# Kernel optimization log

Measured on AMD Instinct MI355X. Metric: run time of the kernel, lower is better.

## Reference

```python
import jax, jax.numpy as jnp
import numpy as np

K = 10
ALPHA = 0.1
N_NODES = 100000
N_EDGES = 1600000
D_FEAT = 50


def setup_inputs() -> dict:
    key = jax.random.key(0)
    k1, k2, k3 = jax.random.split(key, 3)
    feat = jax.random.normal(k1, (N_NODES, D_FEAT), dtype=jnp.float32)
    src = jax.random.randint(k2, (N_EDGES,), 0, N_NODES, dtype=jnp.int64)
    dst = jax.random.randint(k3, (N_EDGES,), 0, N_NODES, dtype=jnp.int64)
    return {"feat": feat, "src": src, "dst": dst}


def reference(feat, src, dst):
    # APPNP: H^{t+1} = (1-a) * D^{-1/2} A D^{-1/2} H^t + a * H^0
    n = feat.shape[0]
    # in-degree per node, clipped to >= 1 (as in the original clip_by_value)
    deg = jax.ops.segment_sum(jnp.ones(dst.shape[0], feat.dtype), dst, num_segments=n)
    norm = jnp.clip(deg, 1.0, None) ** -0.5  # [N]
    norm = norm[:, None]                      # broadcast over feature dims
    feat_0 = feat
    for _ in range(K):
        h = feat * norm                       # pre-normalize (D^{-1/2})
        # message = h[src] (edge weight is 1 since edge_drop=0), aggregate by sum at dst
        agg = jax.ops.segment_sum(h[src], dst, num_segments=n)  # [N, D]
        feat = (1.0 - ALPHA) * (agg * norm) + ALPHA * feat_0
    return feat
```

## Files before the change

kernel.cpp:

```cpp
#include <hip/hip_runtime.h>


#define NN 100000
#define EE 1600000
#define DD 50
#define GS 64
#define KK 10
#define NBLK 391
#define PBLK 256
#define PE (EE / PBLK)
#define PR 4
#define NR (NN / PR)
#define CAP 2176
#define SG 32

__device__ __forceinline__ float feat_at(const void* f, long long i, int ft) {
    if (ft) return ((const float*)f)[i];
    unsigned int w = ((unsigned int)((const unsigned short*)f)[i]) << 16;
    return __uint_as_float(w);
}

__device__ __forceinline__ float bf16_ld(const unsigned short* p, int i) {
    unsigned int w = ((unsigned int)p[i]) << 16;
    return __uint_as_float(w);
}

__device__ __forceinline__ unsigned short bf16_st(float x) {
    unsigned int u = __float_as_uint(x);
    unsigned int r = (u + 0x7FFF + ((u >> 16) & 1)) >> 16;
    return (unsigned short)r;
}

__global__ __launch_bounds__(512) void APPNPConv_62199716381208_build(
        const void* srcp, const void* dstp, const void* featp,
        int2* pairs, int* rcnt, unsigned int* counts,
        int* row_ptr, int* col_idx, int* flag, int phase) {
    __shared__ unsigned int hist[NR / 2];
    __shared__ unsigned int cur[PR];
    const int tid = threadIdx.x;

    if (phase == 0) {
        const int sp = blockIdx.x;
        const long long e0 = (long long)sp * PE;
        const int* a = (const int*)dstp;
        const int is64 = ((a[1] | a[3] | a[5] | a[7] | a[9] | a[11] | a[13] | a[15]) == 0);
        if (sp == 0 && tid == 0) {
            flag[0] = is64;
            const unsigned short* w = (const unsigned short*)featp;
            int isf32 = 0;
            for (int k = 0; k < 64; ++k) {
                unsigned int b = ((unsigned int)w[k]) << 16;
                float ax = fabsf(__uint_as_float(b));
                if (!(ax < 100.0f)) isf32 = 1;
            }
            flag[1] = isf32;
        }
        if (tid < PR) cur[tid] = 0u;
        __syncthreads();
        const int lane = tid & 63;
        const unsigned long long lmask = (1ULL << lane) - 1ULL;
        const long long* dst64 = (const long long*)dstp;
        const long long* src64 = (const long long*)srcp;
        const int* dst32 = (const int*)dstp;
        const int* src32 = (const int*)srcp;
        for (int i = tid; i < PE; i += 512) {
            long long e = e0 + i;
            int d, c;
            if (is64) { d = (int)dst64[e]; c = (int)src64[e]; }
            else      { d = dst32[e];      c = src32[e]; }
            int ok = ((unsigned int)d < (unsigned int)NN);
            int cc = ((unsigned int)c < (unsigned int)NN) ? c : 0;
            int r = ok ? (d / NR) : -1;
            #pragma unroll
            for (int rb = 0; rb < PR; ++rb) {
                unsigned long long m = __ballot(r == rb);
                if (m) {
                    int leader = (int)__ffsll((unsigned long long)m) - 1;
                    unsigned int base = 0u;
                    if (lane == leader)
                        base = atomicAdd(&cur[rb], (unsigned int)__popcll(m));
                    base = (unsigned int)__shfl((int)base, leader, 64);
                    if (r == rb) {
                        unsigned int pos = base + (unsigned int)__popcll(m & lmask);
                        if (pos < (unsigned int)CAP)
                            pairs[((sp << 2) + rb) * CAP + pos] = make_int2(d, cc);
                    }
                }
            }
        }
        __syncthreads();
        if (tid < PR) {
            unsigned int v = cur[tid];
            rcnt[(sp << 2) + tid] = (int)(v < (unsigned int)CAP ? v : (unsigned int)CAP);
        }
        return;
    }

    const int r = blockIdx.x & 3;
    const int sg = blockIdx.x >> 2;

    if (phase == 1) {
        for (int i = tid; i < NR / 2; i += 512) hist[i] = 0u;
        __syncthreads();
        #pragma unroll
        for (int k = 0; k < 8; ++k) {
            int sp = (sg << 3) + k;
            int len = rcnt[(sp << 2) + r];
            const int2* pb = pairs + ((sp << 2) + r) * CAP;
            for (int i = tid; i < len; i += 512) {
                int2 pc = pb[i];
                int dloc = pc.x - r * NR;
                atomicAdd(&hist[dloc >> 1], 1u << ((dloc & 1) << 4));
            }
        }
        __syncthreads();
        for (int i = tid; i < NR; i += 512)
            counts[(size_t)sg * NN + r * NR + i] =
                (hist[i >> 1] >> ((i & 1) << 4)) & 0xFFFFu;
        return;
    }

    {
        const unsigned int* cb = counts + (size_t)sg * NN + r * NR;
        for (int i = tid; i < NR / 2; i += 512) {
            unsigned int lo = cb[2 * i];
            unsigned int hi = cb[2 * i + 1];
            hist[i] = (lo & 0xFFFFu) | (hi << 16);
        }
        __syncthreads();
        #pragma unroll
        for (int k = 0; k < 8; ++k) {
            int sp = (sg << 3) + k;
            int len = rcnt[(sp << 2) + r];
            const int2* pb = pairs + ((sp << 2) + r) * CAP;
            for (int i = tid; i < len; i += 512) {
                int2 pc = pb[i];
                int dloc = pc.x - r * NR;
                unsigned int old = atomicAdd(&hist[dloc >> 1], 1u << ((dloc & 1) << 4));
                unsigned int off = (old >> ((dloc & 1) << 4)) & 0xFFFFu;
                unsigned int pos = (unsigned int)row_ptr[pc.x] + off;
                if (pos < (unsigned int)EE) col_idx[pos] = pc.y;
            }
        }
        return;
    }
}

__global__ __launch_bounds__(512) void APPNPConv_62199716381208_kernel(
        const void* featp, const void* srcp, const void* dstp,
        int* deg, float* norm, int* row_ptr, int* col_idx, int* bsum, int* flag,
        unsigned int* counts,
        const unsigned short* gin, unsigned short* gout, float* outp,
        int phase, int last) {
    __shared__ int sh[512];
    const int tid = threadIdx.x;

    if (phase == 2) {
        int n = blockIdx.x * 256 + tid;
        int total = 0;
        if (n < NN) {
            #pragma unroll 4
            for (int s = 0; s < SG; ++s)
                total += (int)counts[(size_t)s * NN + n];
            deg[n] = total;
            norm[n] = rsqrtf((float)(total < 1 ? 1 : total));
        }
        sh[tid] = total;
        __syncthreads();
        for (int off = 128; off > 0; off >>= 1) {
            if (tid < off) sh[tid] += sh[tid + off];
            __syncthreads();
        }
        if (tid == 0) bsum[blockIdx.x] = sh[0];
        return;
    }
    if (phase == 3) {
        int v = (tid < NBLK) ? bsum[tid] : 0;
        sh[tid] = v;
        __syncthreads();
        for (int off = 1; off < 512; off <<= 1) {
            int x = (tid >= off) ? sh[tid - off] : 0;
            __syncthreads();
            sh[tid] += x;
            __syncthreads();
        }
        if (tid < NBLK) bsum[tid] = sh[tid] - v;
        return;
    }
    if (phase == 4) {
        int i = blockIdx.x * 256 + tid;
        int v = (i < NN) ? deg[i] : 0;
        sh[tid] = v;
        __syncthreads();
        for (int off = 1; off < 256; off <<= 1) {
            int x = (tid >= off) ? sh[tid - off] : 0;
            __syncthreads();
            sh[tid] += x;
            __syncthreads();
        }
        int excl = sh[tid] - v + bsum[blockIdx.x];
        if (i < NN) {
            row_ptr[i] = excl;
            unsigned int run = 0u;
            for (int s = 0; s < SG; ++s) {
                size_t o = (size_t)s * NN + i;
                unsigned int c = counts[o];
                counts[o] = run;
                run += c;
            }
        }
        if (i == 0) row_ptr[NN] = EE;
        return;
    }
    if (phase == 6) {
        int gidx = blockIdx.x * 256 + tid;
        int v = gidx >> 6;
        int d = gidx & 63;
        if (v < NN) {
            unsigned short val = 0;
            if (d < DD) {
                float x = feat_at(featp, (long long)v * DD + d, flag[1]);
                val = bf16_st(x * norm[v]);
            }
            gout[(v << 6) + d] = val;
        }
        return;
    }
    {
        const int lane = tid & 63;
        const int nwg = gridDim.x;
        const int xcd = blockIdx.x & 7;
        const int bpos = blockIdx.x >> 3;
        const int q = nwg >> 3, rm = nwg & 7;
        const int sb = (xcd < rm ? xcd * (q + 1) : rm * (q + 1) + (xcd - rm) * q) + bpos;
        const int v = (sb << 2) + (tid >> 6);
        if (v >= NN) return;
        const int act = (lane < DD);
        float f0 = act ? feat_at(featp, (long long)v * DD + lane, flag[1]) : 0.0f;
        const int beg = row_ptr[v];
        const int end = row_ptr[v + 1];
        float s0 = 0.0f, s1 = 0.0f, s2 = 0.0f, s3 = 0.0f;
        for (int base = beg; base < end; base += 64) {
            int idx = base + lane;
            int my = (idx < end) ? __builtin_nontemporal_load(col_idx + idx) : 0;
            int cnt = end - base;
            if (cnt > 64) cnt = 64;
            int j = 0;
            for (; j + 16 <= cnt; j += 16) {
                int c0  = __shfl(my, j,      64);
                int c1  = __shfl(my, j + 1,  64);
                int c2  = __shfl(my, j + 2,  64);
                int c3  = __shfl(my, j + 3,  64);
                int c4  = __shfl(my, j + 4,  64);
                int c5  = __shfl(my, j + 5,  64);
                int c6  = __shfl(my, j + 6,  64);
                int c7  = __shfl(my, j + 7,  64);
                int c8  = __shfl(my, j + 8,  64);
                int c9  = __shfl(my, j + 9,  64);
                int c10 = __shfl(my, j + 10, 64);
                int c11 = __shfl(my, j + 11, 64);
                int c12 = __shfl(my, j + 12, 64);
                int c13 = __shfl(my, j + 13, 64);
                int c14 = __shfl(my, j + 14, 64);
                int c15 = __shfl(my, j + 15, 64);
                float v0  = bf16_ld(gin, (c0  << 6) + lane);
                float v1  = bf16_ld(gin, (c1  << 6) + lane);
                float v2  = bf16_ld(gin, (c2  << 6) + lane);
                float v3  = bf16_ld(gin, (c3  << 6) + lane);
                float v4  = bf16_ld(gin, (c4  << 6) + lane);
                float v5  = bf16_ld(gin, (c5  << 6) + lane);
                float v6  = bf16_ld(gin, (c6  << 6) + lane);
                float v7  = bf16_ld(gin, (c7  << 6) + lane);
                float v8  = bf16_ld(gin, (c8  << 6) + lane);
                float v9  = bf16_ld(gin, (c9  << 6) + lane);
                float v10 = bf16_ld(gin, (c10 << 6) + lane);
                float v11 = bf16_ld(gin, (c11 << 6) + lane);
                float v12 = bf16_ld(gin, (c12 << 6) + lane);
                float v13 = bf16_ld(gin, (c13 << 6) + lane);
                float v14 = bf16_ld(gin, (c14 << 6) + lane);
                float v15 = bf16_ld(gin, (c15 << 6) + lane);
                s0 += (v0 + v4) + (v8 + v12);
                s1 += (v1 + v5) + (v9 + v13);
                s2 += (v2 + v6) + (v10 + v14);
                s3 += (v3 + v7) + (v11 + v15);
            }
            for (; j + 8 <= cnt; j += 8) {
                int c0 = __shfl(my, j, 64);
                int c1 = __shfl(my, j + 1, 64);
                int c2 = __shfl(my, j + 2, 64);
                int c3 = __shfl(my, j + 3, 64);
                int c4 = __shfl(my, j + 4, 64);
                int c5 = __shfl(my, j + 5, 64);
                int c6 = __shfl(my, j + 6, 64);
                int c7 = __shfl(my, j + 7, 64);
                float v0 = bf16_ld(gin, (c0 << 6) + lane);
                float v1 = bf16_ld(gin, (c1 << 6) + lane);
                float v2 = bf16_ld(gin, (c2 << 6) + lane);
                float v3 = bf16_ld(gin, (c3 << 6) + lane);
                float v4 = bf16_ld(gin, (c4 << 6) + lane);
                float v5 = bf16_ld(gin, (c5 << 6) + lane);
                float v6 = bf16_ld(gin, (c6 << 6) + lane);
                float v7 = bf16_ld(gin, (c7 << 6) + lane);
                s0 += v0 + v4;
                s1 += v1 + v5;
                s2 += v2 + v6;
                s3 += v3 + v7;
            }
            for (; j + 4 <= cnt; j += 4) {
                int c0 = __shfl(my, j, 64);
                int c1 = __shfl(my, j + 1, 64);
                int c2 = __shfl(my, j + 2, 64);
                int c3 = __shfl(my, j + 3, 64);
                s0 += bf16_ld(gin, (c0 << 6) + lane);
                s1 += bf16_ld(gin, (c1 << 6) + lane);
                s2 += bf16_ld(gin, (c2 << 6) + lane);
                s3 += bf16_ld(gin, (c3 << 6) + lane);
            }
            for (; j < cnt; ++j) {
                int c = __shfl(my, j, 64);
                s0 += bf16_ld(gin, (c << 6) + lane);
            }
        }
        float sum = (s0 + s1) + (s2 + s3);
        float nv = norm[v];
        float res = 0.9f * (sum * nv) + 0.1f * f0;
        if (last) {
            if (act) outp[(long long)v * DD + lane] = res;
        } else {
            unsigned short st = act ? bf16_st(res * nv) : (unsigned short)0;
            gout[(v << 6) + lane] = st;
        }
    }
}

extern "C" void kernel_launch(void* const* d_in, const int* in_sizes, int n_in,
                              void* d_out, int out_size, void* d_ws, size_t ws_size,
                              hipStream_t stream) {
    const void* featp = d_in[0];
    const void* src = d_in[1];
    const void* dst = d_in[2];
    float* outf = (float*)d_out;
    unsigned short* P_do = (unsigned short*)d_out;
    int2* pairs = (int2*)d_out;
    size_t out_bytes = (size_t)out_size * 4;
    (void)in_sizes;

    if (n_in != 3) {
        hipMemsetAsync(d_out, 0x50, out_bytes, stream);
        return;
    }

    size_t a_deg  = (((size_t)NN * 4) + 255) / 256 * 256;
    size_t a_norm = a_deg;
    size_t a_rp   = (((size_t)(NN + 1) * 4) + 255) / 256 * 256;
    size_t a_col  = (((size_t)EE * 4) + 255) / 256 * 256;
    size_t a_bsum = (((size_t)NBLK * 4) + 255) / 256 * 256;
    size_t a_flag = 256;
    size_t a_rcnt = (((size_t)PBLK * PR * 4) + 255) / 256 * 256;
    size_t a_buf  = (((size_t)NN * GS * 2) + 255) / 256 * 256;
    if (ws_size < a_deg + a_norm + a_rp + a_col + a_bsum + a_flag + a_rcnt + a_buf ||
        out_bytes < (size_t)PBLK * PR * CAP * 8 ||
        out_bytes < (size_t)NN * GS * 2) {
        hipMemsetAsync(d_out, 0x40, out_bytes, stream);
        return;
    }
    char* p = (char*)d_ws;
    int* deg      = (int*)p;   p += a_deg;
    float* norm   = (float*)p; p += a_norm;
    int* row_ptr  = (int*)p;   p += a_rp;
    int* col_idx  = (int*)p;   p += a_col;
    int* bsum     = (int*)p;   p += a_bsum;
    int* flag     = (int*)p;   p += a_flag;
    int* rcnt     = (int*)p;   p += a_rcnt;
    unsigned short* P_ws = (unsigned short*)p;
    unsigned int* counts = (unsigned int*)p;

    (void)hipGetLastError();

    #define LCH(grid, blk, gi, go, ph, la) \
        APPNPConv_62199716381208_kernel<<<(grid), (blk), 0, stream>>>( \
            featp, src, dst, deg, norm, row_ptr, col_idx, bsum, flag, counts, \
            (gi), (go), outf, (ph), (la))
    #define LCB(grid, ph) \
        APPNPConv_62199716381208_build<<<(grid), 512, 0, stream>>>( \
            src, dst, featp, pairs, rcnt, counts, row_ptr, col_idx, flag, (ph))

    LCB(PBLK, 0);
    LCB(SG * PR, 1);
    LCH(NBLK, 256, P_ws, P_ws, 2, 0);
    LCH(1, 512, P_ws, P_ws, 3, 0);
    LCH(NBLK, 256, P_ws, P_ws, 4, 0);
    LCB(SG * PR, 2);
    LCH((NN * GS + 255) / 256, 256, P_ws, P_do, 6, 0);

    for (int it = 1; it <= KK; ++it) {
        const unsigned short* gi = (it & 1) ? P_do : P_ws;
        unsigned short* go       = (it & 1) ? P_ws : P_do;
        LCH(NN / 4, 256, gi, go, 7, (it == KK) ? 1 : 0);
    }
    #undef LCH
    #undef LCB

    if (hipGetLastError() != hipSuccess) {
        hipMemsetAsync(d_out, 0xBF, out_bytes, stream);
    }
}
```

Before: 691.9 us.

## Process source rows in synchronized phases per wavefront to improve gather locality

Adds a preprocessing phase that reorders each row's column indices by source-node stripe (eight stripes of 12500 nodes). The propagation kernel now has each wavefront handle 13 destination nodes and walk the stripes in eight passes separated by block barriers, so the gathers of concurrently running waves hit the same part of the bf16 feature table and get better cache reuse. It also drops the XCD block remapping, loads f0 with nontemporal loads, and sends rows with more than 64 neighbours to a simple fallback loop. The costs are lower parallelism (1924 blocks instead of 25000), a serial per-edge inner loop without the earlier unrolling, extra barrier stalls, and one more kernel launch.

```diff
diff --git a/kernel.cpp b/kernel.cpp
--- a/kernel.cpp
+++ b/kernel.cpp
@@ -13,10 +13,20 @@
 #define NR (NN / PR)
 #define CAP 2176
 #define SG 32
+#define NPW 13
+#define GBLK 1924
+#define STRW 12500
 
 __device__ __forceinline__ float feat_at(const void* f, long long i, int ft) {
     if (ft) return ((const float*)f)[i];
     unsigned int w = ((unsigned int)((const unsigned short*)f)[i]) << 16;
+    return __uint_as_float(w);
+}
+
+__device__ __forceinline__ float feat_nt(const void* f, long long i, int ft) {
+    if (ft) return __builtin_nontemporal_load((const float*)f + i);
+    unsigned int w = ((unsigned int)__builtin_nontemporal_load(
+                         (const unsigned short*)f + i)) << 16;
     return __uint_as_float(w);
 }
 
@@ -212,6 +222,27 @@
         if (i == 0) row_ptr[NN] = EE;
         return;
     }
+    if (phase == 5) {
+        const int lane = tid & 63;
+        const int v = (blockIdx.x << 2) + (tid >> 6);
+        if (v >= NN) return;
+        int b = row_ptr[v];
+        int e = row_ptr[v + 1];
+        int dg = e - b;
+        if (dg <= 1 || dg > 64) return;
+        int c = (lane < dg) ? col_idx[b + lane] : 0;
+        int key = (lane < dg) ? (c / STRW) : 8;
+        unsigned long long lmask = (1ULL << lane) - 1ULL;
+        int base = 0, rank = 0;
+        #pragma unroll
+        for (int bb = 0; bb < 8; ++bb) {
+            unsigned long long m = __ballot(key == bb);
+            if (key == bb) rank = base + (int)__popcll(m & lmask);
+            base += (int)__popcll(m);
+        }
+        if (lane < dg) col_idx[b + rank] = c;
+        return;
+    }
     if (phase == 6) {
         int gidx = blockIdx.x * 256 + tid;
         int v = gidx >> 6;
@@ -228,107 +259,78 @@
     }
     {
         const int lane = tid & 63;
-        const int nwg = gridDim.x;
-        const int xcd = blockIdx.x & 7;
-        const int bpos = blockIdx.x >> 3;
-        const int q = nwg >> 3, rm = nwg & 7;
-        const int sb = (xcd < rm ? xcd * (q + 1) : rm * (q + 1) + (xcd - rm) * q) + bpos;
-        const int v = (sb << 2) + (tid >> 6);
-        if (v >= NN) return;
+        const int wgl = (blockIdx.x << 2) + (tid >> 6);
+        const int v0 = wgl * NPW;
         const int act = (lane < DD);
-        float f0 = act ? feat_at(featp, (long long)v * DD + lane, flag[1]) : 0.0f;
-        const int beg = row_ptr[v];
-        const int end = row_ptr[v + 1];
-        float s0 = 0.0f, s1 = 0.0f, s2 = 0.0f, s3 = 0.0f;
-        for (int base = beg; base < end; base += 64) {
-            int idx = base + lane;
-            int my = (idx < end) ? __builtin_nontemporal_load(col_idx + idx) : 0;
-            int cnt = end - base;
-            if (cnt > 64) cnt = 64;
-            int j = 0;
-            for (; j + 16 <= cnt; j += 16) {
-                int c0  = __shfl(my, j,      64);
-                int c1  = __shfl(my, j + 1,  64);
-                int c2  = __shfl(my, j + 2,  64);
-                int c3  = __shfl(my, j + 3,  64);
-                int c4  = __shfl(my, j + 4,  64);
-                int c5  = __shfl(my, j + 5,  64);
-                int c6  = __shfl(my, j + 6,  64);
-                int c7  = __shfl(my, j + 7,  64);
-                int c8  = __shfl(my, j + 8,  64);
-                int c9  = __shfl(my, j + 9,  64);
-                int c10 = __shfl(my, j + 10, 64);
-                int c11 = __shfl(my, j + 11, 64);
-                int c12 = __shfl(my, j + 12, 64);
-                int c13 = __shfl(my, j + 13, 64);
-                int c14 = __shfl(my, j + 14, 64);
-                int c15 = __shfl(my, j + 15, 64);
-                float v0  = bf16_ld(gin, (c0  << 6) + lane);
-                float v1  = bf16_ld(gin, (c1  << 6) + lane);
-                float v2  = bf16_ld(gin, (c2  << 6) + lane);
-                float v3  = bf16_ld(gin, (c3  << 6) + lane);
-                float v4  = bf16_ld(gin, (c4  << 6) + lane);
-                float v5  = bf16_ld(gin, (c5  << 6) + lane);
-                float v6  = bf16_ld(gin, (c6  << 6) + lane);
-                float v7  = bf16_ld(gin, (c7  << 6) + lane);
-                float v8  = bf16_ld(gin, (c8  << 6) + lane);
-                float v9  = bf16_ld(gin, (c9  << 6) + lane);
-                float v10 = bf16_ld(gin, (c10 << 6) + lane);
-                float v11 = bf16_ld(gin, (c11 << 6) + lane);
-                float v12 = bf16_ld(gin, (c12 << 6) + lane);
-                float v13 = bf16_ld(gin, (c13 << 6) + lane);
-                float v14 = bf16_ld(gin, (c14 << 6) + lane);
-                float v15 = bf16_ld(gin, (c15 << 6) + lane);
-                s0 += (v0 + v4) + (v8 + v12);
-                s1 += (v1 + v5) + (v9 + v13);
-                s2 += (v2 + v6) + (v10 + v14);
-                s3 += (v3 + v7) + (v11 + v15);
-            }
-            for (; j + 8 <= cnt; j += 8) {
-                int c0 = __shfl(my, j, 64);
-                int c1 = __shfl(my, j + 1, 64);
-                int c2 = __shfl(my, j + 2, 64);
-                int c3 = __shfl(my, j + 3, 64);
-                int c4 = __shfl(my, j + 4, 64);
-                int c5 = __shfl(my, j + 5, 64);
-                int c6 = __shfl(my, j + 6, 64);
-                int c7 = __shfl(my, j + 7, 64);
-                float v0 = bf16_ld(gin, (c0 << 6) + lane);
-                float v1 = bf16_ld(gin, (c1 << 6) + lane);
-                float v2 = bf16_ld(gin, (c2 << 6) + lane);
-                float v3 = bf16_ld(gin, (c3 << 6) + lane);
-                float v4 = bf16_ld(gin, (c4 << 6) + lane);
-                float v5 = bf16_ld(gin, (c5 << 6) + lane);
-                float v6 = bf16_ld(gin, (c6 << 6) + lane);
-                float v7 = bf16_ld(gin, (c7 << 6) + lane);
-                s0 += v0 + v4;
-                s1 += v1 + v5;
-                s2 += v2 + v6;
-                s3 += v3 + v7;
-            }
-            for (; j + 4 <= cnt; j += 4) {
-                int c0 = __shfl(my, j, 64);
-                int c1 = __shfl(my, j + 1, 64);
-                int c2 = __shfl(my, j + 2, 64);
-                int c3 = __shfl(my, j + 3, 64);
-                s0 += bf16_ld(gin, (c0 << 6) + lane);
-                s1 += bf16_ld(gin, (c1 << 6) + lane);
-                s2 += bf16_ld(gin, (c2 << 6) + lane);
-                s3 += bf16_ld(gin, (c3 << 6) + lane);
-            }
-            for (; j < cnt; ++j) {
-                int c = __shfl(my, j, 64);
-                s0 += bf16_ld(gin, (c << 6) + lane);
-            }
-        }
-        float sum = (s0 + s1) + (s2 + s3);
-        float nv = norm[v];
-        float res = 0.9f * (sum * nv) + 0.1f * f0;
-        if (last) {
-            if (act) outp[(long long)v * DD + lane] = res;
-        } else {
-            unsigned short st = act ? bf16_st(res * nv) : (unsigned short)0;
-            gout[(v << 6) + lane] = st;
+        const int ft = flag[1];
+
+        int rl = 0;
+        {
+            int idx = v0 + lane;
+            if (idx > NN) idx = NN;
+            if (lane <= NPW && v0 < NN) rl = row_ptr[idx];
+        }
+        int degr[NPW], my[NPW];
+        float acc[NPW];
+        #pragma unroll
+        for (int n = 0; n < NPW; ++n) {
+            int b = __shfl(rl, n, 64);
+            int e = __shfl(rl, n + 1, 64);
+            int valid = (v0 + n < NN) && (v0 < NN);
+            degr[n] = valid ? (e - b) : 0;
+            acc[n] = 0.0f;
+            int idx = b + lane;
+            my[n] = (degr[n] > 0 && idx < EE) ? col_idx[idx] : 0;
+        }
+        #pragma unroll
+        for (int n = 0; n < NPW; ++n) {
+            if (degr[n] > 64) {
+                int v = v0 + n;
+                int b = row_ptr[v];
+                int e = row_ptr[v + 1];
+                for (int base = b; base < e; base += 64) {
+                    int idx = base + lane;
+                    int mw = (idx < e) ? col_idx[idx] : 0;
+                    int cnt = e - base; if (cnt > 64) cnt = 64;
+                    for (int j = 0; j < cnt; ++j) {
+                        int cc = __shfl(mw, j, 64);
+                        acc[n] += bf16_ld(gin, (cc << 6) + lane);
+                    }
+                }
+            }
+        }
+        for (int p = 0; p < 8; ++p) {
+            #pragma unroll
+            for (int n = 0; n < NPW; ++n) {
+                int dg = degr[n];
+                if (dg == 0 || dg > 64) continue;
+                int k = (lane < dg) ? (my[n] / STRW) : 8;
+                unsigned long long mlo = __ballot(k < p);
+                unsigned long long mcu = __ballot(k == p);
+                int lo = (int)__popcll(mlo);
+                int hi = lo + (int)__popcll(mcu);
+                for (int j = lo; j < hi; ++j) {
+                    int cc = __shfl(my[n], j, 64);
+                    acc[n] += bf16_ld(gin, (cc << 6) + lane);
+                }
+            }
+            __syncthreads();
+        }
+        float nl = 0.0f;
+        if (lane < NPW && v0 + lane < NN) nl = norm[v0 + lane];
+        #pragma unroll
+        for (int n = 0; n < NPW; ++n) {
+            int v = v0 + n;
+            if (v >= NN) continue;
+            float nv = __shfl(nl, n, 64);
+            float f0 = act ? feat_nt(featp, (long long)v * DD + lane, ft) : 0.0f;
+            float res = 0.9f * (acc[n] * nv) + 0.1f * f0;
+            if (last) {
+                if (act) outp[(long long)v * DD + lane] = res;
+            } else {
+                unsigned short st = act ? bf16_st(res * nv) : (unsigned short)0;
+                gout[(v << 6) + lane] = st;
+            }
         }
     }
 }
@@ -391,12 +393,13 @@
     LCH(1, 512, P_ws, P_ws, 3, 0);
     LCH(NBLK, 256, P_ws, P_ws, 4, 0);
     LCB(SG * PR, 2);
+    LCH(NN / 4, 256, P_ws, P_ws, 5, 0);
     LCH((NN * GS + 255) / 256, 256, P_ws, P_do, 6, 0);
 
     for (int it = 1; it <= KK; ++it) {
         const unsigned short* gi = (it & 1) ? P_do : P_ws;
         unsigned short* go       = (it & 1) ? P_ws : P_do;
-        LCH(NN / 4, 256, gi, go, 7, (it == KK) ? 1 : 0);
+        LCH(GBLK, 256, gi, go, 7, (it == KK) ? 1 : 0);
     }
     #undef LCH
     #undef LCB
```

Measured after the change: 2.027 ms. 193% more time.
